# Optimization experiments

Measured on AMD Instinct MI355X. Metric: run time of the kernel, lower is better.

## Reference

```python
import jax, jax.numpy as jnp
import numpy as np

BETA = 0.25


def setup_inputs() -> dict:
    key = jax.random.key(0)
    k1, k2 = jax.random.split(key)
    inputs = jax.random.normal(k1, (32, 4096, 64), dtype=jnp.float32)
    # VarianceScaling(uniform) ~ small-magnitude init; plain normal scaled works for a numeric reference
    codebook = jax.random.normal(k2, (1024, 64), dtype=jnp.float32) * (1.0 / np.sqrt(64.0))
    return {"inputs": inputs, "codebook": codebook}


def reference(inputs, codebook):
    D = codebook.shape[-1]
    flat = jnp.reshape(inputs, (-1, D))                      # [N, D]
    flat_sqr = jnp.sum(flat ** 2, axis=-1, keepdims=True)    # [N, 1]
    code_sqr = jnp.sum(codebook ** 2, axis=-1)[None, :]      # [1, K]
    # full pairwise squared distances [N, K]
    distances = flat_sqr - 2.0 * (flat @ codebook.T) + code_sqr
    encoding_indices = jnp.reshape(jnp.argmin(distances, axis=-1), inputs.shape[:-1])
    quantize = codebook[encoding_indices]                    # gather -> [..., D]
    encoding_loss = jnp.mean((jax.lax.stop_gradient(inputs) - quantize) ** 2)
    commit_loss = jnp.mean((inputs - jax.lax.stop_gradient(quantize)) ** 2)
    loss = encoding_loss + BETA * commit_loss
    # straight-through estimator
    z_q = inputs + jax.lax.stop_gradient(quantize - inputs)
    return loss, z_q, encoding_indices
```

## Files before the change

kernel.cpp:

```cpp
#include <hip/hip_runtime.h>

#define N_ROWS 131072
#define D 64
#define K_CODES 1024

typedef _Float16 f16x8 __attribute__((ext_vector_type(8)));
typedef float    f32x4 __attribute__((ext_vector_type(4)));

#define MFMA16(a, b, c) __builtin_amdgcn_mfma_f32_16x16x32_f16((a), (b), (c), 0, 0, 0)

__global__ __launch_bounds__(256)
void prep_kernel(const float* __restrict__ CB, _Float16* __restrict__ CBf,
                 float* __restrict__ csqr, float* __restrict__ loss) {
    const int b = blockIdx.x, t = threadIdx.x;
    if (b < 64) {
        const int unit = b * 256 + t;
        const int tile = unit >> 8;
        const int f    = (unit >> 6) & 3;
        const int lane = unit & 63;
        const int quad = lane >> 4, lrow = lane & 15;
        const int code = tile * 16 + lrow;
        const int k0   = (f & 1) * 32 + quad * 8;
        const float* src = CB + (size_t)code * D + k0;
        float4 v0 = *(const float4*)(src);
        float4 v1 = *(const float4*)(src + 4);
        float xs[8] = {v0.x, v0.y, v0.z, v0.w, v1.x, v1.y, v1.z, v1.w};
        f16x8 o;
#pragma unroll
        for (int j = 0; j < 8; ++j) {
            _Float16 h = (_Float16)xs[j];
            o[j] = (f < 2) ? h : (_Float16)(xs[j] - (float)h);
        }
        *(f16x8*)(CBf + (size_t)unit * 8) = o;
    } else {
        if (t == 0) *loss = 0.0f;
        for (int k = t; k < K_CODES; k += 256) {
            const float4* p = (const float4*)(CB + (size_t)k * D);
            float s = 0.0f;
#pragma unroll
            for (int i = 0; i < 16; ++i) {
                float4 v = p[i];
                s += v.x * v.x + v.y * v.y + v.z * v.z + v.w * v.w;
            }
            csqr[k] = s;
        }
    }
}

__global__ __launch_bounds__(256, 2)
void argmin_kernel(const float* __restrict__ X,
                   const _Float16* __restrict__ CBf,
                   const float* __restrict__ csqr,
                   const float* __restrict__ CB,
                   float* __restrict__ out) {
    __shared__ float LsC[K_CODES];
    __shared__ float candD[128][2];
    __shared__ int   candI[128][2];
    __shared__ int   ivfin[128];
    __shared__ float xsqW[2];
    __shared__ float lossW[2];

    const int t    = threadIdx.x;
    const int wave = t >> 6;
    const int lane = t & 63;
    const int lrow = lane & 15;
    const int quad = lane >> 4;
    const int rh   = wave >> 1;
    const int ch   = wave & 1;
    const int R0   = blockIdx.x * 128;
    const int Rw   = R0 + rh * 64;

    ((float4*)LsC)[t] = ((const float4*)csqr)[t];

    f16x8 Ah[4][2], Al[4][2];
    float xsq = 0.0f;
#pragma unroll
    for (int mt = 0; mt < 4; ++mt) {
        const float* xr = X + (size_t)(Rw + mt * 16 + lrow) * D;
#pragma unroll
        for (int ks = 0; ks < 2; ++ks) {
            const int k0 = ks * 32 + quad * 8;
            float4 v0 = *(const float4*)(xr + k0);
            float4 v1 = *(const float4*)(xr + k0 + 4);
            float xs[8] = {v0.x, v0.y, v0.z, v0.w, v1.x, v1.y, v1.z, v1.w};
            f16x8 h, l;
#pragma unroll
            for (int j = 0; j < 8; ++j) {
                xsq += xs[j] * xs[j];
                float sv = -2.0f * xs[j];
                _Float16 hh = (_Float16)sv;
                h[j] = hh;
                l[j] = (_Float16)(sv - (float)hh);
            }
            Ah[mt][ks] = h;
            Al[mt][ks] = l;
        }
    }
    __syncthreads();

    float bestd[4][4];
    int   besti[4][4];
#pragma unroll
    for (int mt = 0; mt < 4; ++mt)
#pragma unroll
        for (int r = 0; r < 4; ++r) { bestd[mt][r] = 3.0e38f; besti[mt][r] = 0; }

    const f16x8* gw = (const f16x8*)CBf + (size_t)ch * 32 * 256 + lane;

#define ALOAD(Bv, tl)                                                         \
    do {                                                                      \
        const f16x8* _p = gw + (size_t)(tl) * 256;                            \
        asm volatile(                                                         \
            "global_load_dwordx4 %0, %4, off\n\t"                             \
            "global_load_dwordx4 %1, %4, off offset:1024\n\t"                 \
            "global_load_dwordx4 %2, %4, off offset:2048\n\t"                 \
            "global_load_dwordx4 %3, %4, off offset:3072"                     \
            : "=&v"(Bv[0]), "=&v"(Bv[1]), "=&v"(Bv[2]), "=&v"(Bv[3])          \
            : "v"(_p));                                                       \
    } while (0)

#define WAITB(Bv)                                                             \
    asm volatile("s_waitcnt vmcnt(12)"                                        \
                 : "+v"(Bv[0]), "+v"(Bv[1]), "+v"(Bv[2]), "+v"(Bv[3]))

#define COMPUTE(Bv, tl)                                                       \
    do {                                                                      \
        const int   c  = (ch * 32 + (tl)) * 16 + lrow;                        \
        const float cs = LsC[c];                                              \
        _Pragma("unroll")                                                     \
        for (int mt = 0; mt < 4; ++mt) {                                      \
            f32x4 acc = {cs, cs, cs, cs};                                     \
            acc = MFMA16(Ah[mt][0], Bv[0], acc);                              \
            acc = MFMA16(Ah[mt][1], Bv[1], acc);                              \
            acc = MFMA16(Al[mt][0], Bv[0], acc);                              \
            acc = MFMA16(Al[mt][1], Bv[1], acc);                              \
            acc = MFMA16(Ah[mt][0], Bv[2], acc);                              \
            acc = MFMA16(Ah[mt][1], Bv[3], acc);                              \
            _Pragma("unroll")                                                 \
            for (int r = 0; r < 4; ++r) {                                     \
                bool lt = acc[r] < bestd[mt][r];                              \
                bestd[mt][r] = lt ? acc[r] : bestd[mt][r];                    \
                besti[mt][r] = lt ? c : besti[mt][r];                         \
            }                                                                 \
        }                                                                     \
    } while (0)

    f16x8 B0[4], B1[4], B2[4], B3[4];
    ALOAD(B0, 0);
    ALOAD(B1, 1);
    ALOAD(B2, 2);
    for (int tl = 0; tl < 32; tl += 4) {
        ALOAD(B3, (tl + 3) & 31);
        WAITB(B0);
        COMPUTE(B0, tl);
        ALOAD(B0, (tl + 4) & 31);
        WAITB(B1);
        COMPUTE(B1, tl + 1);
        ALOAD(B1, (tl + 5) & 31);
        WAITB(B2);
        COMPUTE(B2, tl + 2);
        ALOAD(B2, (tl + 6) & 31);
        WAITB(B3);
        COMPUTE(B3, tl + 3);
    }
    asm volatile("s_waitcnt vmcnt(0)"
                 :
                 : "v"(B0[0]), "v"(B0[1]), "v"(B0[2]), "v"(B0[3]),
                   "v"(B1[0]), "v"(B1[1]), "v"(B1[2]), "v"(B1[3]),
                   "v"(B2[0]), "v"(B2[1]), "v"(B2[2]), "v"(B2[3]),
                   "v"(B3[0]), "v"(B3[1]), "v"(B3[2]), "v"(B3[3])
                 : "memory");

    if (ch == 0) {
        float s = xsq;
#pragma unroll
        for (int m = 1; m < 64; m <<= 1) s += __shfl_xor(s, m, 64);
        if (lane == 0) xsqW[rh] = s;
    }

#pragma unroll
    for (int mt = 0; mt < 4; ++mt) {
#pragma unroll
        for (int r = 0; r < 4; ++r) {
            float dv = bestd[mt][r];
            int   iv = besti[mt][r];
#pragma unroll
            for (int m = 1; m < 16; m <<= 1) {
                float od = __shfl_xor(dv, m, 64);
                int   oi = __shfl_xor(iv, m, 64);
                if (od < dv || (od == dv && oi < iv)) { dv = od; iv = oi; }
            }
            if (lrow == 0) {
                int rl = rh * 64 + mt * 16 + quad * 4 + r;
                candD[rl][ch] = dv;
                candI[rl][ch] = iv;
            }
        }
    }
    __syncthreads();

    const float scale = 1.25f / (float)((size_t)N_ROWS * D);
    if (t < 128) {
        float d0 = candD[t][0], d1 = candD[t][1];
        int   i0 = candI[t][0], i1 = candI[t][1];
        bool take1 = d1 < d0;
        float dv = take1 ? d1 : d0;
        int   iv = take1 ? i1 : i0;
        out[1 + (size_t)N_ROWS * D + R0 + t] = (float)iv;
        ivfin[t] = iv;
        float ssum = dv;
#pragma unroll
        for (int m = 1; m < 64; m <<= 1) ssum += __shfl_xor(ssum, m, 64);
        if (lane == 0) lossW[wave] = ssum;
    }
    __syncthreads();
    if (t == 0)
        atomicAdd(out, (lossW[0] + lossW[1] + xsqW[0] + xsqW[1]) * scale);

    float* p = out + 1 + (size_t)R0 * D;
#pragma unroll
    for (int i = 0; i < 8; ++i) {
        int q = i * 256 + t;
        int j = 4 * q + 3;
        if (q < 2047) {
            float v[4];
#pragma unroll
            for (int e = 0; e < 4; ++e) {
                int jj = j + e;
                v[e] = CB[(size_t)ivfin[jj >> 6] * D + (jj & 63)];
            }
            *(float4*)(p + j) = make_float4(v[0], v[1], v[2], v[3]);
        } else if (q == 2047) {
            p[8191] = CB[(size_t)ivfin[127] * D + 63];
        }
    }
    if (t == 0) {
        const float* c0 = CB + (size_t)ivfin[0] * D;
        p[0] = c0[0];
        p[1] = c0[1];
        p[2] = c0[2];
    }
}

extern "C" void kernel_launch(void* const* d_in, const int* in_sizes, int n_in,
                              void* d_out, int out_size, void* d_ws,
                              size_t ws_size, hipStream_t stream) {
    const float* X  = (const float*)d_in[0];
    const float* CB = (const float*)d_in[1];

    float*    csqr = (float*)d_ws;
    _Float16* CBf  = (_Float16*)((char*)d_ws + 4096);

    hipLaunchKernelGGL(prep_kernel, dim3(65), dim3(256), 0, stream,
                       CB, CBf, csqr, (float*)d_out);
    hipLaunchKernelGGL(argmin_kernel, dim3(N_ROWS / 128), dim3(256), 0, stream,
                       X, CBf, csqr, CB, (float*)d_out);
}
```

Before: 152.5 us.

## Keep codebook slices resident in registers and stream input rows through waves

Each of 8 waves now holds its 128-code slice of the split-fp16 codebook (with the -2 scale folded in during prep) in registers for the whole block. The block streams 512 input rows in 16-row chunks, and every 128 rows it reduces candidates across waves in shared memory and writes indices and quantized outputs. This removes the per-row-tile reloading of the codebook from global memory and the software-pipelined loads. In exchange it needs many more registers per thread and adds extra __syncthreads per 128-row group. Input-row loads are no longer prefetched, so their latency sits directly on the MFMA path.

```diff
diff --git a/kernel.cpp b/kernel.cpp
--- a/kernel.cpp
+++ b/kernel.cpp
@@ -28,8 +28,9 @@
         f16x8 o;
 #pragma unroll
         for (int j = 0; j < 8; ++j) {
-            _Float16 h = (_Float16)xs[j];
-            o[j] = (f < 2) ? h : (_Float16)(xs[j] - (float)h);
+            float sv = -2.0f * xs[j];
+            _Float16 h = (_Float16)sv;
+            o[j] = (f < 2) ? h : (_Float16)(sv - (float)h);
         }
         *(f16x8*)(CBf + (size_t)unit * 8) = o;
     } else {
@@ -47,36 +48,45 @@
     }
 }
 
-__global__ __launch_bounds__(256, 2)
+__global__ __launch_bounds__(512, 2)
 void argmin_kernel(const float* __restrict__ X,
                    const _Float16* __restrict__ CBf,
                    const float* __restrict__ csqr,
                    const float* __restrict__ CB,
                    float* __restrict__ out) {
-    __shared__ float LsC[K_CODES];
-    __shared__ float candD[128][2];
-    __shared__ int   candI[128][2];
+    __shared__ float candD[128][9];
+    __shared__ int   candI[128][9];
     __shared__ int   ivfin[128];
-    __shared__ float xsqW[2];
-    __shared__ float lossW[2];
+    __shared__ float lsum[4][2];
 
     const int t    = threadIdx.x;
     const int wave = t >> 6;
     const int lane = t & 63;
+    const int quad = lane >> 4;
     const int lrow = lane & 15;
-    const int quad = lane >> 4;
-    const int rh   = wave >> 1;
-    const int ch   = wave & 1;
-    const int R0   = blockIdx.x * 128;
-    const int Rw   = R0 + rh * 64;
-
-    ((float4*)LsC)[t] = ((const float4*)csqr)[t];
-
-    f16x8 Ah[4][2], Al[4][2];
+    const int Rb   = blockIdx.x * 512;
+
+    f16x8 Bt[8][4];
+    {
+        const f16x8* gb = (const f16x8*)CBf + (size_t)(wave * 8) * 256 + lane;
+#pragma unroll
+        for (int tt = 0; tt < 8; ++tt)
+#pragma unroll
+            for (int f = 0; f < 4; ++f)
+                Bt[tt][f] = gb[tt * 256 + f * 64];
+    }
+    float csqrR[8];
+#pragma unroll
+    for (int tt = 0; tt < 8; ++tt)
+        csqrR[tt] = csqr[wave * 128 + tt * 16 + lrow];
+    const int codeB = wave * 128 + lrow;
+
     float xsq = 0.0f;
-#pragma unroll
-    for (int mt = 0; mt < 4; ++mt) {
-        const float* xr = X + (size_t)(Rw + mt * 16 + lrow) * D;
+    const float scale = 1.25f / (float)((size_t)N_ROWS * D);
+
+    for (int c = 0; c < 32; ++c) {
+        const float* xr = X + (size_t)(Rb + c * 16 + lrow) * D;
+        f16x8 Ah[2], Al[2];
 #pragma unroll
         for (int ks = 0; ks < 2; ++ks) {
             const int k0 = ks * 32 + quad * 8;
@@ -87,103 +97,52 @@
 #pragma unroll
             for (int j = 0; j < 8; ++j) {
                 xsq += xs[j] * xs[j];
-                float sv = -2.0f * xs[j];
-                _Float16 hh = (_Float16)sv;
+                _Float16 hh = (_Float16)xs[j];
                 h[j] = hh;
-                l[j] = (_Float16)(sv - (float)hh);
-            }
-            Ah[mt][ks] = h;
-            Al[mt][ks] = l;
-        }
-    }
-    __syncthreads();
-
-    float bestd[4][4];
-    int   besti[4][4];
-#pragma unroll
-    for (int mt = 0; mt < 4; ++mt)
-#pragma unroll
-        for (int r = 0; r < 4; ++r) { bestd[mt][r] = 3.0e38f; besti[mt][r] = 0; }
-
-    const f16x8* gw = (const f16x8*)CBf + (size_t)ch * 32 * 256 + lane;
-
-#define ALOAD(Bv, tl)                                                         \
-    do {                                                                      \
-        const f16x8* _p = gw + (size_t)(tl) * 256;                            \
-        asm volatile(                                                         \
-            "global_load_dwordx4 %0, %4, off\n\t"                             \
-            "global_load_dwordx4 %1, %4, off offset:1024\n\t"                 \
-            "global_load_dwordx4 %2, %4, off offset:2048\n\t"                 \
-            "global_load_dwordx4 %3, %4, off offset:3072"                     \
-            : "=&v"(Bv[0]), "=&v"(Bv[1]), "=&v"(Bv[2]), "=&v"(Bv[3])          \
-            : "v"(_p));                                                       \
-    } while (0)
-
-#define WAITB(Bv)                                                             \
-    asm volatile("s_waitcnt vmcnt(12)"                                        \
-                 : "+v"(Bv[0]), "+v"(Bv[1]), "+v"(Bv[2]), "+v"(Bv[3]))
-
-#define COMPUTE(Bv, tl)                                                       \
-    do {                                                                      \
-        const int   c  = (ch * 32 + (tl)) * 16 + lrow;                        \
-        const float cs = LsC[c];                                              \
-        _Pragma("unroll")                                                     \
-        for (int mt = 0; mt < 4; ++mt) {                                      \
-            f32x4 acc = {cs, cs, cs, cs};                                     \
-            acc = MFMA16(Ah[mt][0], Bv[0], acc);                              \
-            acc = MFMA16(Ah[mt][1], Bv[1], acc);                              \
-            acc = MFMA16(Al[mt][0], Bv[0], acc);                              \
-            acc = MFMA16(Al[mt][1], Bv[1], acc);                              \
-            acc = MFMA16(Ah[mt][0], Bv[2], acc);                              \
-            acc = MFMA16(Ah[mt][1], Bv[3], acc);                              \
-            _Pragma("unroll")                                                 \
-            for (int r = 0; r < 4; ++r) {                                     \
-                bool lt = acc[r] < bestd[mt][r];                              \
-                bestd[mt][r] = lt ? acc[r] : bestd[mt][r];                    \
-                besti[mt][r] = lt ? c : besti[mt][r];                         \
-            }                                                                 \
-        }                                                                     \
-    } while (0)
-
-    f16x8 B0[4], B1[4], B2[4], B3[4];
-    ALOAD(B0, 0);
-    ALOAD(B1, 1);
-    ALOAD(B2, 2);
-    for (int tl = 0; tl < 32; tl += 4) {
-        ALOAD(B3, (tl + 3) & 31);
-        WAITB(B0);
-        COMPUTE(B0, tl);
-        ALOAD(B0, (tl + 4) & 31);
-        WAITB(B1);
-        COMPUTE(B1, tl + 1);
-        ALOAD(B1, (tl + 5) & 31);
-        WAITB(B2);
-        COMPUTE(B2, tl + 2);
-        ALOAD(B2, (tl + 6) & 31);
-        WAITB(B3);
-        COMPUTE(B3, tl + 3);
-    }
-    asm volatile("s_waitcnt vmcnt(0)"
-                 :
-                 : "v"(B0[0]), "v"(B0[1]), "v"(B0[2]), "v"(B0[3]),
-                   "v"(B1[0]), "v"(B1[1]), "v"(B1[2]), "v"(B1[3]),
-                   "v"(B2[0]), "v"(B2[1]), "v"(B2[2]), "v"(B2[3]),
-                   "v"(B3[0]), "v"(B3[1]), "v"(B3[2]), "v"(B3[3])
-                 : "memory");
-
-    if (ch == 0) {
-        float s = xsq;
-#pragma unroll
-        for (int m = 1; m < 64; m <<= 1) s += __shfl_xor(s, m, 64);
-        if (lane == 0) xsqW[rh] = s;
-    }
-
-#pragma unroll
-    for (int mt = 0; mt < 4; ++mt) {
+                l[j] = (_Float16)(xs[j] - (float)hh);
+            }
+            Ah[ks] = h;
+            Al[ks] = l;
+        }
+
+        f32x4 acc[8];
+#pragma unroll
+        for (int tt = 0; tt < 8; ++tt) {
+            float cs = csqrR[tt];
+            acc[tt] = (f32x4){cs, cs, cs, cs};
+        }
+#pragma unroll
+        for (int tt = 0; tt < 8; ++tt) acc[tt] = MFMA16(Ah[0], Bt[tt][0], acc[tt]);
+#pragma unroll
+        for (int tt = 0; tt < 8; ++tt) acc[tt] = MFMA16(Ah[1], Bt[tt][1], acc[tt]);
+#pragma unroll
+        for (int tt = 0; tt < 8; ++tt) acc[tt] = MFMA16(Al[0], Bt[tt][0], acc[tt]);
+#pragma unroll
+        for (int tt = 0; tt < 8; ++tt) acc[tt] = MFMA16(Al[1], Bt[tt][1], acc[tt]);
+#pragma unroll
+        for (int tt = 0; tt < 8; ++tt) acc[tt] = MFMA16(Ah[0], Bt[tt][2], acc[tt]);
+#pragma unroll
+        for (int tt = 0; tt < 8; ++tt) acc[tt] = MFMA16(Ah[1], Bt[tt][3], acc[tt]);
+
+        float bd[4];
+        int   bi[4];
+#pragma unroll
+        for (int r = 0; r < 4; ++r) { bd[r] = acc[0][r]; bi[r] = codeB; }
+#pragma unroll
+        for (int tt = 1; tt < 8; ++tt) {
+            const int cc = codeB + tt * 16;
+#pragma unroll
+            for (int r = 0; r < 4; ++r) {
+                bool lt = acc[tt][r] < bd[r];
+                bd[r] = lt ? acc[tt][r] : bd[r];
+                bi[r] = lt ? cc : bi[r];
+            }
+        }
+
 #pragma unroll
         for (int r = 0; r < 4; ++r) {
-            float dv = bestd[mt][r];
-            int   iv = besti[mt][r];
+            float dv = bd[r];
+            int   iv = bi[r];
 #pragma unroll
             for (int m = 1; m < 16; m <<= 1) {
                 float od = __shfl_xor(dv, m, 64);
@@ -191,54 +150,70 @@
                 if (od < dv || (od == dv && oi < iv)) { dv = od; iv = oi; }
             }
             if (lrow == 0) {
-                int rl = rh * 64 + mt * 16 + quad * 4 + r;
-                candD[rl][ch] = dv;
-                candI[rl][ch] = iv;
-            }
-        }
-    }
-    __syncthreads();
-
-    const float scale = 1.25f / (float)((size_t)N_ROWS * D);
-    if (t < 128) {
-        float d0 = candD[t][0], d1 = candD[t][1];
-        int   i0 = candI[t][0], i1 = candI[t][1];
-        bool take1 = d1 < d0;
-        float dv = take1 ? d1 : d0;
-        int   iv = take1 ? i1 : i0;
-        out[1 + (size_t)N_ROWS * D + R0 + t] = (float)iv;
-        ivfin[t] = iv;
-        float ssum = dv;
-#pragma unroll
-        for (int m = 1; m < 64; m <<= 1) ssum += __shfl_xor(ssum, m, 64);
-        if (lane == 0) lossW[wave] = ssum;
-    }
-    __syncthreads();
-    if (t == 0)
-        atomicAdd(out, (lossW[0] + lossW[1] + xsqW[0] + xsqW[1]) * scale);
-
-    float* p = out + 1 + (size_t)R0 * D;
-#pragma unroll
-    for (int i = 0; i < 8; ++i) {
-        int q = i * 256 + t;
-        int j = 4 * q + 3;
-        if (q < 2047) {
-            float v[4];
-#pragma unroll
-            for (int e = 0; e < 4; ++e) {
-                int jj = j + e;
-                v[e] = CB[(size_t)ivfin[jj >> 6] * D + (jj & 63)];
-            }
-            *(float4*)(p + j) = make_float4(v[0], v[1], v[2], v[3]);
-        } else if (q == 2047) {
-            p[8191] = CB[(size_t)ivfin[127] * D + 63];
-        }
-    }
-    if (t == 0) {
-        const float* c0 = CB + (size_t)ivfin[0] * D;
-        p[0] = c0[0];
-        p[1] = c0[1];
-        p[2] = c0[2];
+                int rl = (c & 7) * 16 + quad * 4 + r;
+                candD[rl][wave] = dv;
+                candI[rl][wave] = iv;
+            }
+        }
+
+        if ((c & 7) == 7) {
+            __syncthreads();
+            const int g = c >> 3;
+            if (t < 128) {
+                float dv = candD[t][0];
+                int   iv = candI[t][0];
+#pragma unroll
+                for (int w = 1; w < 8; ++w) {
+                    float od = candD[t][w];
+                    bool  lt = od < dv;
+                    iv = lt ? candI[t][w] : iv;
+                    dv = lt ? od : dv;
+                }
+                ivfin[t] = iv;
+                out[1 + (size_t)N_ROWS * D + Rb + g * 128 + t] = (float)iv;
+                float s = dv;
+#pragma unroll
+                for (int m = 1; m < 64; m <<= 1) s += __shfl_xor(s, m, 64);
+                if (lane == 0) lsum[g][t >> 6] = s;
+            }
+            __syncthreads();
+            float* p = out + 1 + (size_t)(Rb + g * 128) * D;
+#pragma unroll
+            for (int i = 0; i < 4; ++i) {
+                int q = i * 512 + t;
+                int j = 4 * q + 3;
+                if (q < 2047) {
+                    float v[4];
+#pragma unroll
+                    for (int e = 0; e < 4; ++e) {
+                        int jj = j + e;
+                        v[e] = CB[(size_t)ivfin[jj >> 6] * D + (jj & 63)];
+                    }
+                    *(float4*)(p + j) = make_float4(v[0], v[1], v[2], v[3]);
+                } else if (q == 2047) {
+                    p[8191] = CB[(size_t)ivfin[127] * D + 63];
+                }
+            }
+            if (t == 0) {
+                const float* c0 = CB + (size_t)ivfin[0] * D;
+                p[0] = c0[0];
+                p[1] = c0[1];
+                p[2] = c0[2];
+            }
+            __syncthreads();
+        }
+    }
+
+    if (wave == 0) {
+        float s = xsq;
+#pragma unroll
+        for (int m = 1; m < 64; m <<= 1) s += __shfl_xor(s, m, 64);
+        if (lane == 0) {
+            float L = s;
+#pragma unroll
+            for (int g = 0; g < 4; ++g) L += lsum[g][0] + lsum[g][1];
+            atomicAdd(out, L * scale);
+        }
     }
 }
 
@@ -253,6 +228,6 @@
 
     hipLaunchKernelGGL(prep_kernel, dim3(65), dim3(256), 0, stream,
                        CB, CBf, csqr, (float*)d_out);
-    hipLaunchKernelGGL(argmin_kernel, dim3(N_ROWS / 128), dim3(256), 0, stream,
+    hipLaunchKernelGGL(argmin_kernel, dim3(N_ROWS / 512), dim3(512), 0, stream,
                        X, CBf, csqr, CB, (float*)d_out);
 }
```

Result: slower. 217.6 us (+42.7%).
